# Kernel optimization log

Measured on AMD Instinct MI355X. Metric: run time of the kernel, lower is better.

The kernel has to match this reference:

```python
import jax, jax.numpy as jnp
import numpy as np

D_MODEL, D_STATE, D_CONV, EXPAND = 1024, 16, 4, 2
D_INNER = EXPAND * D_MODEL
B, L = 1, 2048
LN_EPS = 1e-5


def setup_inputs() -> dict:
    key = jax.random.key(0)
    ks = jax.random.split(key, 10)
    s = lambda fan_in: 1.0 / np.sqrt(fan_in)
    return {
        "x": jax.random.normal(ks[0], (B, L, D_MODEL), dtype=jnp.float32),
        "in_proj_w": jax.random.uniform(ks[1], (2 * D_INNER, D_MODEL), jnp.float32, -s(D_MODEL), s(D_MODEL)),
        "conv_w": jax.random.uniform(ks[2], (D_INNER, 1, D_CONV), jnp.float32, -s(D_CONV), s(D_CONV)),
        "conv_b": jax.random.uniform(ks[3], (D_INNER,), jnp.float32, -s(D_CONV), s(D_CONV)),
        "x_proj_w": jax.random.uniform(ks[4], (2 * D_STATE + 1, D_INNER), jnp.float32, -s(D_INNER), s(D_INNER)),
        "dt_w": jax.random.uniform(ks[5], (D_INNER,), jnp.float32, -1.0, 1.0),
        "dt_b": jax.random.uniform(ks[6], (D_INNER,), jnp.float32, -1.0, 1.0),
        "A_log": jnp.log(jnp.broadcast_to(jnp.arange(1, D_STATE + 1, dtype=jnp.float32), (D_INNER, D_STATE))),
        "D": jnp.ones((D_INNER,), jnp.float32),
        "out_proj_w": jax.random.uniform(ks[7], (D_MODEL, D_INNER), jnp.float32, -s(D_INNER), s(D_INNER)),
        "ln_g": jnp.ones((D_MODEL,), jnp.float32),
        "ln_b": jnp.zeros((D_MODEL,), jnp.float32),
    }


def _layernorm(x, g, b):
    mu = jnp.mean(x, axis=-1, keepdims=True)
    var = jnp.var(x, axis=-1, keepdims=True)
    return (x - mu) * jax.lax.rsqrt(var + LN_EPS) * g + b


def _selective_scan(xc, delta, A, Bm, Cm, Dp):
    # xc,delta: (B,L,D); A: (D,N); Bm,Cm: (B,L,N); Dp: (D,)
    deltaA = jnp.exp(delta[..., None] * A)                 # (B,L,D,N)
    deltaBx = delta[..., None] * Bm[:, :, None, :] * xc[..., None]  # (B,L,D,N)
    h0 = jnp.zeros((xc.shape[0], xc.shape[2], A.shape[1]), xc.dtype)

    def step(h, inp):
        dA_t, dBx_t, c_t = inp                             # (B,D,N),(B,D,N),(B,N)
        h = dA_t * h + dBx_t
        y_t = jnp.einsum('bdn,bn->bd', h, c_t)
        return h, y_t

    xs = (jnp.swapaxes(deltaA, 0, 1), jnp.swapaxes(deltaBx, 0, 1), jnp.swapaxes(Cm, 0, 1))
    _, ys = jax.lax.scan(step, h0, xs)                     # ys: (L,B,D)
    y = jnp.swapaxes(ys, 0, 1)
    return y + xc * Dp


def reference(x, in_proj_w, conv_w, conv_b, x_proj_w, dt_w, dt_b, A_log, D, out_proj_w, ln_g, ln_b):
    residual = x
    xn = _layernorm(x, ln_g, ln_b)
    xz = jnp.einsum('bld,ed->ble', xn, in_proj_w)          # (B,L,2*D_INNER)
    x_proj, z = jnp.split(xz, 2, axis=-1)
    # depthwise causal conv1d (torch pads d_conv-1 both sides then truncates to L == left-pad only)
    lhs = jnp.swapaxes(x_proj, 1, 2)                       # (B,D,L)
    xc = jax.lax.conv_general_dilated(
        lhs, conv_w, window_strides=(1,), padding=[(D_CONV - 1, 0)],
        dimension_numbers=('NCH', 'OIH', 'NCH'), feature_group_count=D_INNER)
    xc = jnp.swapaxes(xc + conv_b[None, :, None], 1, 2)    # (B,L,D)
    xc = jax.nn.silu(xc)
    x_ssm = jnp.einsum('bld,ed->ble', xc, x_proj_w)        # (B,L,2N+1)
    dt, Bm, Cm = jnp.split(x_ssm, [1, 1 + D_STATE], axis=-1)
    delta = jax.nn.softplus(dt * dt_w + dt_b)              # (B,L,1)*(D,) -> (B,L,D)
    A = -jnp.exp(A_log.astype(jnp.float32))
    y = _selective_scan(xc, delta, A, Bm, Cm, D)
    y = y * jax.nn.silu(z)
    out = jnp.einsum('bld,ed->ble', y, out_proj_w)
    return out + residual
```

## Files before the change

### kernel.cpp

```cpp
#include <hip/hip_runtime.h>
#include <hip/hip_bf16.h>

#define L_SEQ 2048
#define DM    1024
#define DI    2048
#define NST   16
#define NC    64
#define LC    (L_SEQ/NC)
#define KSPLIT 16
#define KCH   (DI/KSPLIT)
#define KS_OUT 4

typedef __bf16 bf16x8 __attribute__((ext_vector_type(8)));
typedef float  f32x4  __attribute__((ext_vector_type(4)));
typedef unsigned short u16x4 __attribute__((ext_vector_type(4)));

__device__ inline unsigned short f2bf(float f){
  __hip_bfloat16 h = __float2bfloat16(f);
  return *reinterpret_cast<unsigned short*>(&h);
}

__device__ inline void gload16(const void* g, void* l){
  __builtin_amdgcn_global_load_lds(
      (const __attribute__((address_space(1))) void*)g,
      (__attribute__((address_space(3))) void*)l, 16, 0, 0);
}

__global__ __launch_bounds__(256) void ln_kernel(
    const float* __restrict__ x, const float* __restrict__ g,
    const float* __restrict__ b, __hip_bfloat16* __restrict__ xn)
{
  int t = blockIdx.x, tid = threadIdx.x;
  const float4 v = ((const float4*)(x + (size_t)t*DM))[tid];
  float s  = v.x+v.y+v.z+v.w;
  float ss = v.x*v.x+v.y*v.y+v.z*v.z+v.w*v.w;
  #pragma unroll
  for (int m=1;m<64;m<<=1){ s += __shfl_xor(s,m); ss += __shfl_xor(ss,m); }
  __shared__ float sb[4], ssb[4];
  if ((tid&63)==0){ sb[tid>>6]=s; ssb[tid>>6]=ss; }
  __syncthreads();
  s  = sb[0]+sb[1]+sb[2]+sb[3];
  ss = ssb[0]+ssb[1]+ssb[2]+ssb[3];
  float mu  = s*(1.f/DM);
  float var = ss*(1.f/DM) - mu*mu;
  float rs  = rsqrtf(var + 1e-5f);
  float4 gg = ((const float4*)g)[tid], bb = ((const float4*)b)[tid];
  u16x4 o = { f2bf((v.x-mu)*rs*gg.x+bb.x), f2bf((v.y-mu)*rs*gg.y+bb.y),
              f2bf((v.z-mu)*rs*gg.z+bb.z), f2bf((v.w-mu)*rs*gg.w+bb.w) };
  *(u16x4*)((unsigned short*)xn + (size_t)t*DM + tid*4) = o;
}

__global__ __launch_bounds__(256) void cvt_bf16(
    const float* __restrict__ in, __hip_bfloat16* __restrict__ out, int n)
{
  int i = (blockIdx.x*256 + threadIdx.x)*4;
  if (i >= n) return;
  float4 v = *(const float4*)(in+i);
  u16x4 o = { f2bf(v.x), f2bf(v.y), f2bf(v.z), f2bf(v.w) };
  *(u16x4*)((unsigned short*)out + i) = o;
}

template<int EPI>
__global__ __launch_bounds__(256) void gemm_bt(
    const __hip_bfloat16* __restrict__ A, const __hip_bfloat16* __restrict__ B,
    void* __restrict__ Cout, int M, int N, int K)
{
  __shared__ __align__(16) unsigned short As[2][128*64];
  __shared__ __align__(16) unsigned short Bs[2][128*64];
  int tid = threadIdx.x;
  int w = tid>>6, l = tid&63;
  int m0 = blockIdx.y*128, n0 = blockIdx.x*128;
  int wr = (w>>1)*64, wc = (w&1)*64;
  int lr = l&15, lk = l>>4;
  int kchunk = K/gridDim.z;
  int kbase = blockIdx.z*kchunk;
  int ktiles = kchunk/64;
  f32x4 acc[4][4] = {};

  int cbase = w*64 + l;
  auto stage = [&](int buf, int k0){
    #pragma unroll
    for (int i=0;i<4;i++){
      int cc = i*256 + cbase;
      int row = cc>>3, q = cc&7;
      gload16(A + (size_t)(m0+row)*K + k0 + q*8, (char*)&As[buf][0] + (size_t)(i*256 + w*64)*16);
      gload16(B + (size_t)(n0+row)*K + k0 + q*8, (char*)&Bs[buf][0] + (size_t)(i*256 + w*64)*16);
    }
  };

  stage(0, kbase);
  __syncthreads();
  int cur = 0;
  for (int kt=0; kt<ktiles; ++kt){
    if (kt+1 < ktiles) stage(cur^1, kbase + (kt+1)*64);
    #pragma unroll
    for (int kk=0;kk<2;kk++){
      bf16x8 af[4], bfb[4];
      #pragma unroll
      for (int i=0;i<4;i++){
        af[i]  = *(const bf16x8*)&As[cur][(wr + i*16 + lr)*64 + kk*32 + lk*8];
        bfb[i] = *(const bf16x8*)&Bs[cur][(wc + i*16 + lr)*64 + kk*32 + lk*8];
      }
      #pragma unroll
      for (int i=0;i<4;i++)
        #pragma unroll
        for (int j=0;j<4;j++)
          acc[i][j] = __builtin_amdgcn_mfma_f32_16x16x32_bf16(af[i], bfb[j], acc[i][j], 0,0,0);
    }
    if (kt+1 < ktiles){ __syncthreads(); cur ^= 1; }
  }

  float* Cb = (float*)Cout + (size_t)blockIdx.z*M*N;
  #pragma unroll
  for (int i=0;i<4;i++){
    #pragma unroll
    for (int j=0;j<4;j++){
      #pragma unroll
      for (int r=0;r<4;r++){
        int row = m0 + wr + i*16 + lk*4 + r;
        int col = n0 + wc + j*16 + lr;
        Cb[(size_t)row*N + col] = acc[i][j][r];
      }
    }
  }
}

__global__ __launch_bounds__(256) void reduce_res(
    const float* __restrict__ part, const float* __restrict__ R,
    float* __restrict__ out, int n)
{
  size_t i = (size_t)(blockIdx.x*256 + threadIdx.x)*4;
  if (i >= (size_t)n) return;
  float4 a = *(const float4*)(part + i);
  float4 b = *(const float4*)(part + (size_t)n + i);
  float4 c = *(const float4*)(part + 2*(size_t)n + i);
  float4 d = *(const float4*)(part + 3*(size_t)n + i);
  float4 r = *(const float4*)(R + i);
  float4 o = { a.x+b.x+c.x+d.x+r.x, a.y+b.y+c.y+d.y+r.y,
               a.z+b.z+c.z+d.z+r.z, a.w+b.w+c.w+d.w+r.w };
  *(float4*)(out + i) = o;
}

__global__ __launch_bounds__(256) void conv_silu(
    const float* __restrict__ xz, const float* __restrict__ cw,
    const float* __restrict__ cb, float* __restrict__ xc)
{
  int idx = blockIdx.x*256 + threadIdx.x;
  int t = idx >> 11, d = idx & (DI-1);
  float acc = cb[d];
  #pragma unroll
  for (int j=0;j<4;j++){
    int tt = t - 3 + j;
    if (tt >= 0) acc += xz[(size_t)tt*(2*DI) + d] * cw[d*4 + j];
  }
  xc[idx] = acc / (1.f + __expf(-acc));
}

__global__ __launch_bounds__(256) void gemm2_kernel(
    const float* __restrict__ xc, const float* __restrict__ xpw,
    float* __restrict__ part)
{
  __shared__ float Xs[16*68];
  __shared__ float Ws[33*68];
  int tid = threadIdx.x;
  int t0 = blockIdx.x*16;
  int kbase = blockIdx.y*KCH;
  int tt = tid&15, g = tid>>4;
  float a0=0.f, a1=0.f, a2=0.f;
  for (int k0=kbase; k0<kbase+KCH; k0+=64){
    __syncthreads();
    {
      int ct = tid>>4, kq = tid&15;
      float4 v = *(const float4*)&xc[(size_t)(t0+ct)*DI + k0 + kq*4];
      *(float4*)&Xs[ct*68 + kq*4] = v;
    }
    for (int i=tid; i<528; i+=256){
      int e = i>>4, kq = i&15;
      float4 v = *(const float4*)&xpw[(size_t)e*DI + k0 + kq*4];
      *(float4*)&Ws[e*68 + kq*4] = v;
    }
    __syncthreads();
    #pragma unroll 4
    for (int kq=0;kq<16;kq++){
      float4 xv = *(const float4*)&Xs[tt*68 + kq*4];
      float4 w0 = *(const float4*)&Ws[g*68 + kq*4];
      float4 w1 = *(const float4*)&Ws[(g+16)*68 + kq*4];
      a0 += xv.x*w0.x + xv.y*w0.y + xv.z*w0.z + xv.w*w0.w;
      a1 += xv.x*w1.x + xv.y*w1.y + xv.z*w1.z + xv.w*w1.w;
      if (g==0){
        float4 w2 = *(const float4*)&Ws[32*68 + kq*4];
        a2 += xv.x*w2.x + xv.y*w2.y + xv.z*w2.z + xv.w*w2.w;
      }
    }
  }
  size_t base = (size_t)blockIdx.y*L_SEQ*33 + (size_t)(t0+tt)*33;
  part[base + g]      = a0;
  part[base + g + 16] = a1;
  if (g==0) part[base + 32] = a2;
}

__global__ __launch_bounds__(256) void gemm2_reduce(
    const float* __restrict__ part, float* __restrict__ xssm)
{
  int i = blockIdx.x*256 + threadIdx.x;
  if (i >= L_SEQ*33) return;
  float s = 0.f;
  #pragma unroll
  for (int c=0;c<KSPLIT;c++) s += part[(size_t)c*L_SEQ*33 + i];
  xssm[i] = s;
}

__global__ __launch_bounds__(256) void scan1(
    const float* __restrict__ xssm, float* __restrict__ xc,
    const float* __restrict__ dtw, const float* __restrict__ dtb,
    const float* __restrict__ Alog, const float* __restrict__ Dp,
    float* __restrict__ xz, float* __restrict__ hpart)
{
  int d = blockIdx.x*256 + threadIdx.x;
  int c = blockIdx.y;
  float A[16];
  {
    #pragma unroll
    for (int q=0;q<4;q++){
      float4 al = *(const float4*)&Alog[d*16 + q*4];
      A[q*4+0] = -__expf(al.x); A[q*4+1] = -__expf(al.y);
      A[q*4+2] = -__expf(al.z); A[q*4+3] = -__expf(al.w);
    }
  }
  float wd = dtw[d], bd = dtb[d], Dd = Dp[d];
  float h[16];
  #pragma unroll
  for (int n=0;n<16;n++) h[n] = 0.f;
  float cum = 0.f;
  int t0 = c*LC;
  for (int t=t0; t<t0+LC; ++t){
    const float* row = xssm + (size_t)t*33;
    float dtv = row[0];
    float xv  = xc[(size_t)t*DI + d];
    float u = fmaf(dtv, wd, bd);
    float delta = (u > 20.f) ? u : __logf(1.f + __expf(u));
    cum += delta;
    xc[(size_t)t*DI + d] = cum;
    float dx = delta * xv;
    float y  = Dd * xv;
    #pragma unroll
    for (int n=0;n<16;n++){
      float dA = __expf(delta * A[n]);
      h[n] = fmaf(dA, h[n], row[1+n]*dx);
      y = fmaf(h[n], row[17+n], y);
    }
    xz[(size_t)t*2*DI + d] = y;
  }
  #pragma unroll
  for (int n=0;n<16;n++)
    hpart[((size_t)c*16 + n)*DI + d] = h[n];
}

__global__ __launch_bounds__(256) void scanfix(
    const float* __restrict__ hpart, const float* __restrict__ cumd,
    const float* __restrict__ Alog, float* __restrict__ hinit)
{
  int gid = blockIdx.x*256 + threadIdx.x;
  int d = gid & (DI-1), n = gid >> 11;
  float A = -__expf(Alog[d*16 + n]);
  float h = 0.f;
  for (int c=0;c<NC;c++){
    hinit[((size_t)c*16 + n)*DI + d] = h;
    float E = __expf(A * cumd[(size_t)((c+1)*LC - 1)*DI + d]);
    h = E*h + hpart[((size_t)c*16 + n)*DI + d];
  }
}

__global__ __launch_bounds__(256) void scan2g(
    const float* __restrict__ xssm, const float* __restrict__ cumd,
    const float* __restrict__ hinit, const float* __restrict__ xz,
    const float* __restrict__ Alog, __hip_bfloat16* __restrict__ gb)
{
  int d = blockIdx.x*256 + threadIdx.x;
  int c = blockIdx.y;
  float A[16], h0[16];
  {
    #pragma unroll
    for (int q=0;q<4;q++){
      float4 al = *(const float4*)&Alog[d*16 + q*4];
      A[q*4+0] = -__expf(al.x); A[q*4+1] = -__expf(al.y);
      A[q*4+2] = -__expf(al.z); A[q*4+3] = -__expf(al.w);
    }
  }
  #pragma unroll
  for (int n=0;n<16;n++) h0[n] = hinit[((size_t)c*16 + n)*DI + d];
  int t0 = c*LC;
  for (int t=t0; t<t0+LC; ++t){
    const float* row = xssm + (size_t)t*33;
    float cd = cumd[(size_t)t*DI + d];
    float corr = 0.f;
    #pragma unroll
    for (int n=0;n<16;n++)
      corr = fmaf(__expf(A[n]*cd)*h0[n], row[17+n], corr);
    float y = xz[(size_t)t*2*DI + d] + corr;
    float z = xz[(size_t)t*2*DI + DI + d];
    float s = z / (1.f + __expf(-z));
    gb[(size_t)t*DI + d] = __float2bfloat16(y*s);
  }
}

extern "C" void kernel_launch(void* const* d_in, const int* in_sizes, int n_in,
                              void* d_out, int out_size, void* d_ws, size_t ws_size,
                              hipStream_t stream)
{
  const float* x    = (const float*)d_in[0];
  const float* w_in = (const float*)d_in[1];
  const float* cw   = (const float*)d_in[2];
  const float* cb   = (const float*)d_in[3];
  const float* xpw  = (const float*)d_in[4];
  const float* dtw  = (const float*)d_in[5];
  const float* dtb  = (const float*)d_in[6];
  const float* Alog = (const float*)d_in[7];
  const float* Dp   = (const float*)d_in[8];
  const float* w_out= (const float*)d_in[9];
  const float* lng  = (const float*)d_in[10];
  const float* lnb  = (const float*)d_in[11];
  float* out = (float*)d_out;

  char* p = (char*)d_ws;
  auto carve = [&](size_t bytes)->char*{ char* r = p; p += (bytes + 255) & ~(size_t)255; return r; };
  __hip_bfloat16* xn  = (__hip_bfloat16*)carve((size_t)L_SEQ*DM*2);
  __hip_bfloat16* w1b = (__hip_bfloat16*)carve((size_t)2*DI*DM*2);
  __hip_bfloat16* w3b = (__hip_bfloat16*)carve((size_t)DM*DI*2);
  float* xz   = (float*)carve((size_t)L_SEQ*2*DI*4);
  float* xc   = (float*)carve((size_t)L_SEQ*DI*4);
  float* xssm = (float*)carve((size_t)L_SEQ*33*4);
  float* hpart= (float*)carve((size_t)NC*NST*DI*4);
  float* hinit= (float*)carve((size_t)NC*NST*DI*4);
  __hip_bfloat16* gb = (__hip_bfloat16*)w1b;
  float* part = hpart;
  float* opart = xz;

  ln_kernel<<<L_SEQ, 256, 0, stream>>>(x, lng, lnb, xn);
  cvt_bf16<<<(2*DI*DM)/1024, 256, 0, stream>>>(w_in, w1b, 2*DI*DM);
  cvt_bf16<<<(DM*DI)/1024, 256, 0, stream>>>(w_out, w3b, DM*DI);
  gemm_bt<0><<<dim3((2*DI)/128, L_SEQ/128, 1), 256, 0, stream>>>(xn, w1b, xz, L_SEQ, 2*DI, DM);
  conv_silu<<<(L_SEQ*DI)/256, 256, 0, stream>>>(xz, cw, cb, xc);
  gemm2_kernel<<<dim3(L_SEQ/16, KSPLIT), 256, 0, stream>>>(xc, xpw, part);
  gemm2_reduce<<<(L_SEQ*33 + 255)/256, 256, 0, stream>>>(part, xssm);
  scan1<<<dim3(DI/256, NC), 256, 0, stream>>>(xssm, xc, dtw, dtb, Alog, Dp, xz, hpart);
  scanfix<<<(DI*NST)/256, 256, 0, stream>>>(hpart, xc, Alog, hinit);
  scan2g<<<dim3(DI/256, NC), 256, 0, stream>>>(xssm, xc, hinit, xz, Alog, gb);
  gemm_bt<0><<<dim3(DM/128, L_SEQ/128, KS_OUT), 256, 0, stream>>>(gb, w3b, opart, L_SEQ, DM, DI);
  reduce_res<<<(L_SEQ*DM)/1024, 256, 0, stream>>>(opart, x, out, L_SEQ*DM);
}
```

Before: 170.6 us.

## Fuse conv+SiLU into consumers, recompute delta in scan2, merge weight casts, swizzle GEMM blocks

Removes the standalone conv_silu kernel and the xc buffer. The depthwise conv and SiLU are now recomputed inside gemm2 and scan1 from xz with a sliding window. scan2g recomputes the softplus delta and its running sum instead of reading a stored cumulative-delta array, and scan1 writes only per-chunk end sums plus a separate ylocal buffer. The two weight-cast launches merge into one, and gemm_bt remaps block IDs in groups of 8. Together these cut launches and full-size intermediate reads and writes, at the cost of redundant conv and exp/log arithmetic in several kernels.

```diff
diff --git a/kernel.cpp b/kernel.cpp
--- a/kernel.cpp
+++ b/kernel.cpp
@@ -25,6 +25,8 @@
       (const __attribute__((address_space(1))) void*)g,
       (__attribute__((address_space(3))) void*)l, 16, 0, 0);
 }
+
+__device__ inline float silu(float v){ return v/(1.f + __expf(-v)); }
 
 __global__ __launch_bounds__(256) void ln_kernel(
     const float* __restrict__ x, const float* __restrict__ g,
@@ -50,17 +52,21 @@
   *(u16x4*)((unsigned short*)xn + (size_t)t*DM + tid*4) = o;
 }
 
-__global__ __launch_bounds__(256) void cvt_bf16(
-    const float* __restrict__ in, __hip_bfloat16* __restrict__ out, int n)
+__global__ __launch_bounds__(256) void cvt_weights(
+    const float* __restrict__ w1, const float* __restrict__ w2,
+    __hip_bfloat16* __restrict__ o1, __hip_bfloat16* __restrict__ o2)
 {
   int i = (blockIdx.x*256 + threadIdx.x)*4;
-  if (i >= n) return;
-  float4 v = *(const float4*)(in+i);
+  const int n1 = 2*DI*DM;
+  const float* src; unsigned short* dst; int j;
+  if (i < n1){ src = w1; dst = (unsigned short*)o1; j = i; }
+  else       { src = w2; dst = (unsigned short*)o2; j = i - n1; }
+  float4 v = *(const float4*)(src + j);
   u16x4 o = { f2bf(v.x), f2bf(v.y), f2bf(v.z), f2bf(v.w) };
-  *(u16x4*)((unsigned short*)out + i) = o;
-}
-
-template<int EPI>
+  *(u16x4*)(dst + j) = o;
+}
+
+template<int TAG>
 __global__ __launch_bounds__(256) void gemm_bt(
     const __hip_bfloat16* __restrict__ A, const __hip_bfloat16* __restrict__ B,
     void* __restrict__ Cout, int M, int N, int K)
@@ -69,7 +75,11 @@
   __shared__ __align__(16) unsigned short Bs[2][128*64];
   int tid = threadIdx.x;
   int w = tid>>6, l = tid&63;
-  int m0 = blockIdx.y*128, n0 = blockIdx.x*128;
+  int nwg = gridDim.x*gridDim.y;
+  int bid = blockIdx.y*gridDim.x + blockIdx.x;
+  int cpx = nwg>>3;
+  int nb  = (bid&7)*cpx + (bid>>3);
+  int m0 = (nb/gridDim.x)*128, n0 = (nb%gridDim.x)*128;
   int wr = (w>>1)*64, wc = (w&1)*64;
   int lr = l&15, lk = l>>4;
   int kchunk = K/gridDim.z;
@@ -141,23 +151,9 @@
   *(float4*)(out + i) = o;
 }
 
-__global__ __launch_bounds__(256) void conv_silu(
+__global__ __launch_bounds__(256) void gemm2_kernel(
     const float* __restrict__ xz, const float* __restrict__ cw,
-    const float* __restrict__ cb, float* __restrict__ xc)
-{
-  int idx = blockIdx.x*256 + threadIdx.x;
-  int t = idx >> 11, d = idx & (DI-1);
-  float acc = cb[d];
-  #pragma unroll
-  for (int j=0;j<4;j++){
-    int tt = t - 3 + j;
-    if (tt >= 0) acc += xz[(size_t)tt*(2*DI) + d] * cw[d*4 + j];
-  }
-  xc[idx] = acc / (1.f + __expf(-acc));
-}
-
-__global__ __launch_bounds__(256) void gemm2_kernel(
-    const float* __restrict__ xc, const float* __restrict__ xpw,
+    const float* __restrict__ cb, const float* __restrict__ xpw,
     float* __restrict__ part)
 {
   __shared__ float Xs[16*68];
@@ -171,7 +167,27 @@
     __syncthreads();
     {
       int ct = tid>>4, kq = tid&15;
-      float4 v = *(const float4*)&xc[(size_t)(t0+ct)*DI + k0 + kq*4];
+      int t = t0+ct, k = k0+kq*4;
+      float4 c0 = *(const float4*)&cw[(k+0)*4];
+      float4 c1 = *(const float4*)&cw[(k+1)*4];
+      float4 c2 = *(const float4*)&cw[(k+2)*4];
+      float4 bb = *(const float4*)&cb[k];
+      float4 c3 = *(const float4*)&cw[(k+3)*4];
+      float s0=bb.x, s1=bb.y, s2=bb.z, s3=bb.w;
+      #pragma unroll
+      for (int j=0;j<4;j++){
+        int tj = t-3+j;
+        if (tj >= 0){
+          float4 xv = *(const float4*)&xz[(size_t)tj*2*DI + k];
+          float w0 = (j==0)?c0.x:(j==1)?c0.y:(j==2)?c0.z:c0.w;
+          float w1 = (j==0)?c1.x:(j==1)?c1.y:(j==2)?c1.z:c1.w;
+          float w2 = (j==0)?c2.x:(j==1)?c2.y:(j==2)?c2.z:c2.w;
+          float w3 = (j==0)?c3.x:(j==1)?c3.y:(j==2)?c3.z:c3.w;
+          s0 = fmaf(xv.x, w0, s0); s1 = fmaf(xv.y, w1, s1);
+          s2 = fmaf(xv.z, w2, s2); s3 = fmaf(xv.w, w3, s3);
+        }
+      }
+      float4 v = { silu(s0), silu(s1), silu(s2), silu(s3) };
       *(float4*)&Xs[ct*68 + kq*4] = v;
     }
     for (int i=tid; i<528; i+=256){
@@ -211,36 +227,45 @@
 }
 
 __global__ __launch_bounds__(256) void scan1(
-    const float* __restrict__ xssm, float* __restrict__ xc,
+    const float* __restrict__ xssm, const float* __restrict__ xz,
+    const float* __restrict__ cw, const float* __restrict__ cb,
     const float* __restrict__ dtw, const float* __restrict__ dtb,
     const float* __restrict__ Alog, const float* __restrict__ Dp,
-    float* __restrict__ xz, float* __restrict__ hpart)
+    float* __restrict__ ylocal, float* __restrict__ hpart,
+    float* __restrict__ cend)
 {
   int d = blockIdx.x*256 + threadIdx.x;
   int c = blockIdx.y;
   float A[16];
-  {
-    #pragma unroll
-    for (int q=0;q<4;q++){
-      float4 al = *(const float4*)&Alog[d*16 + q*4];
-      A[q*4+0] = -__expf(al.x); A[q*4+1] = -__expf(al.y);
-      A[q*4+2] = -__expf(al.z); A[q*4+3] = -__expf(al.w);
-    }
-  }
+  #pragma unroll
+  for (int q=0;q<4;q++){
+    float4 al = *(const float4*)&Alog[d*16 + q*4];
+    A[q*4+0] = -__expf(al.x); A[q*4+1] = -__expf(al.y);
+    A[q*4+2] = -__expf(al.z); A[q*4+3] = -__expf(al.w);
+  }
+  float4 cwv = *(const float4*)&cw[d*4];
+  float cbv = cb[d];
   float wd = dtw[d], bd = dtb[d], Dd = Dp[d];
   float h[16];
   #pragma unroll
   for (int n=0;n<16;n++) h[n] = 0.f;
   float cum = 0.f;
   int t0 = c*LC;
+  float xw0=0.f, xw1=0.f, xw2=0.f;
+  if (t0 > 0){
+    xw0 = xz[(size_t)(t0-3)*2*DI + d];
+    xw1 = xz[(size_t)(t0-2)*2*DI + d];
+    xw2 = xz[(size_t)(t0-1)*2*DI + d];
+  }
   for (int t=t0; t<t0+LC; ++t){
     const float* row = xssm + (size_t)t*33;
-    float dtv = row[0];
-    float xv  = xc[(size_t)t*DI + d];
-    float u = fmaf(dtv, wd, bd);
+    float xin = xz[(size_t)t*2*DI + d];
+    float cv = fmaf(xin, cwv.w, fmaf(xw2, cwv.z, fmaf(xw1, cwv.y, fmaf(xw0, cwv.x, cbv))));
+    xw0=xw1; xw1=xw2; xw2=xin;
+    float xv = silu(cv);
+    float u = fmaf(row[0], wd, bd);
     float delta = (u > 20.f) ? u : __logf(1.f + __expf(u));
     cum += delta;
-    xc[(size_t)t*DI + d] = cum;
     float dx = delta * xv;
     float y  = Dd * xv;
     #pragma unroll
@@ -249,15 +274,16 @@
       h[n] = fmaf(dA, h[n], row[1+n]*dx);
       y = fmaf(h[n], row[17+n], y);
     }
-    xz[(size_t)t*2*DI + d] = y;
+    ylocal[(size_t)t*DI + d] = y;
   }
   #pragma unroll
   for (int n=0;n<16;n++)
     hpart[((size_t)c*16 + n)*DI + d] = h[n];
+  cend[(size_t)c*DI + d] = cum;
 }
 
 __global__ __launch_bounds__(256) void scanfix(
-    const float* __restrict__ hpart, const float* __restrict__ cumd,
+    const float* __restrict__ hpart, const float* __restrict__ cend,
     const float* __restrict__ Alog, float* __restrict__ hinit)
 {
   int gid = blockIdx.x*256 + threadIdx.x;
@@ -266,41 +292,55 @@
   float h = 0.f;
   for (int c=0;c<NC;c++){
     hinit[((size_t)c*16 + n)*DI + d] = h;
-    float E = __expf(A * cumd[(size_t)((c+1)*LC - 1)*DI + d]);
+    float E = __expf(A * cend[(size_t)c*DI + d]);
     h = E*h + hpart[((size_t)c*16 + n)*DI + d];
   }
 }
 
 __global__ __launch_bounds__(256) void scan2g(
-    const float* __restrict__ xssm, const float* __restrict__ cumd,
-    const float* __restrict__ hinit, const float* __restrict__ xz,
-    const float* __restrict__ Alog, __hip_bfloat16* __restrict__ gb)
+    const float* __restrict__ xssm, const float* __restrict__ xz,
+    const float* __restrict__ cw, const float* __restrict__ cb,
+    const float* __restrict__ dtw, const float* __restrict__ dtb,
+    const float* __restrict__ Alog, const float* __restrict__ hinit,
+    const float* __restrict__ ylocal, __hip_bfloat16* __restrict__ gb)
 {
   int d = blockIdx.x*256 + threadIdx.x;
   int c = blockIdx.y;
   float A[16], h0[16];
-  {
-    #pragma unroll
-    for (int q=0;q<4;q++){
-      float4 al = *(const float4*)&Alog[d*16 + q*4];
-      A[q*4+0] = -__expf(al.x); A[q*4+1] = -__expf(al.y);
-      A[q*4+2] = -__expf(al.z); A[q*4+3] = -__expf(al.w);
-    }
+  #pragma unroll
+  for (int q=0;q<4;q++){
+    float4 al = *(const float4*)&Alog[d*16 + q*4];
+    A[q*4+0] = -__expf(al.x); A[q*4+1] = -__expf(al.y);
+    A[q*4+2] = -__expf(al.z); A[q*4+3] = -__expf(al.w);
   }
   #pragma unroll
   for (int n=0;n<16;n++) h0[n] = hinit[((size_t)c*16 + n)*DI + d];
+  float4 cwv = *(const float4*)&cw[d*4];
+  float cbv = cb[d];
+  float wd = dtw[d], bd = dtb[d];
+  float cum = 0.f;
   int t0 = c*LC;
+  float xw0=0.f, xw1=0.f, xw2=0.f;
+  if (t0 > 0){
+    xw0 = xz[(size_t)(t0-3)*2*DI + d];
+    xw1 = xz[(size_t)(t0-2)*2*DI + d];
+    xw2 = xz[(size_t)(t0-1)*2*DI + d];
+  }
   for (int t=t0; t<t0+LC; ++t){
     const float* row = xssm + (size_t)t*33;
-    float cd = cumd[(size_t)t*DI + d];
+    float xin = xz[(size_t)t*2*DI + d];
+    float cv = fmaf(xin, cwv.w, fmaf(xw2, cwv.z, fmaf(xw1, cwv.y, fmaf(xw0, cwv.x, cbv))));
+    xw0=xw1; xw1=xw2; xw2=xin;
+    float u = fmaf(row[0], wd, bd);
+    float delta = (u > 20.f) ? u : __logf(1.f + __expf(u));
+    cum += delta;
     float corr = 0.f;
     #pragma unroll
     for (int n=0;n<16;n++)
-      corr = fmaf(__expf(A[n]*cd)*h0[n], row[17+n], corr);
-    float y = xz[(size_t)t*2*DI + d] + corr;
+      corr = fmaf(__expf(A[n]*cum)*h0[n], row[17+n], corr);
+    float y = ylocal[(size_t)t*DI + d] + corr;
     float z = xz[(size_t)t*2*DI + DI + d];
-    float s = z / (1.f + __expf(-z));
-    gb[(size_t)t*DI + d] = __float2bfloat16(y*s);
+    gb[(size_t)t*DI + d] = __float2bfloat16(y*silu(z));
   }
 }
 
@@ -328,24 +368,23 @@
   __hip_bfloat16* w1b = (__hip_bfloat16*)carve((size_t)2*DI*DM*2);
   __hip_bfloat16* w3b = (__hip_bfloat16*)carve((size_t)DM*DI*2);
   float* xz   = (float*)carve((size_t)L_SEQ*2*DI*4);
-  float* xc   = (float*)carve((size_t)L_SEQ*DI*4);
+  float* ylocal=(float*)carve((size_t)L_SEQ*DI*4);
   float* xssm = (float*)carve((size_t)L_SEQ*33*4);
   float* hpart= (float*)carve((size_t)NC*NST*DI*4);
   float* hinit= (float*)carve((size_t)NC*NST*DI*4);
+  float* cend = (float*)carve((size_t)NC*DI*4);
   __hip_bfloat16* gb = (__hip_bfloat16*)w1b;
   float* part = hpart;
   float* opart = xz;
 
   ln_kernel<<<L_SEQ, 256, 0, stream>>>(x, lng, lnb, xn);
-  cvt_bf16<<<(2*DI*DM)/1024, 256, 0, stream>>>(w_in, w1b, 2*DI*DM);
-  cvt_bf16<<<(DM*DI)/1024, 256, 0, stream>>>(w_out, w3b, DM*DI);
+  cvt_weights<<<(2*DI*DM + DM*DI)/1024, 256, 0, stream>>>(w_in, w_out, w1b, w3b);
   gemm_bt<0><<<dim3((2*DI)/128, L_SEQ/128, 1), 256, 0, stream>>>(xn, w1b, xz, L_SEQ, 2*DI, DM);
-  conv_silu<<<(L_SEQ*DI)/256, 256, 0, stream>>>(xz, cw, cb, xc);
-  gemm2_kernel<<<dim3(L_SEQ/16, KSPLIT), 256, 0, stream>>>(xc, xpw, part);
+  gemm2_kernel<<<dim3(L_SEQ/16, KSPLIT), 256, 0, stream>>>(xz, cw, cb, xpw, part);
   gemm2_reduce<<<(L_SEQ*33 + 255)/256, 256, 0, stream>>>(part, xssm);
-  scan1<<<dim3(DI/256, NC), 256, 0, stream>>>(xssm, xc, dtw, dtb, Alog, Dp, xz, hpart);
-  scanfix<<<(DI*NST)/256, 256, 0, stream>>>(hpart, xc, Alog, hinit);
-  scan2g<<<dim3(DI/256, NC), 256, 0, stream>>>(xssm, xc, hinit, xz, Alog, gb);
-  gemm_bt<0><<<dim3(DM/128, L_SEQ/128, KS_OUT), 256, 0, stream>>>(gb, w3b, opart, L_SEQ, DM, DI);
+  scan1<<<dim3(DI/256, NC), 256, 0, stream>>>(xssm, xz, cw, cb, dtw, dtb, Alog, Dp, ylocal, hpart, cend);
+  scanfix<<<(DI*NST)/256, 256, 0, stream>>>(hpart, cend, Alog, hinit);
+  scan2g<<<dim3(DI/256, NC), 256, 0, stream>>>(xssm, xz, cw, cb, dtw, dtb, Alog, hinit, ylocal, gb);
+  gemm_bt<1><<<dim3(DM/128, L_SEQ/128, KS_OUT), 256, 0, stream>>>(gb, w3b, opart, L_SEQ, DM, DI);
   reduce_res<<<(L_SEQ*DM)/1024, 256, 0, stream>>>(opart, x, out, L_SEQ*DM);
 }
```

Result: faster. 163.3 us (-4.3%).
